# Kernel tuning notes

Measured on AMD Instinct MI355X. Metric: run time of the kernel, lower is better.

Reference implementation:

```python
import jax, jax.numpy as jnp
import numpy as np

EMBED_DIM = 1024
NUM_HEADS = 16
HEAD_DIM = EMBED_DIM // NUM_HEADS
B, T = 4, 2048


def setup_inputs() -> dict:
    key = jax.random.key(0)
    ks = jax.random.split(key, 5)
    s = 0.02
    return {
        "x": jax.random.normal(ks[0], (B, T, EMBED_DIM), dtype=jnp.float32),
        "W_qkv": jax.random.normal(ks[1], (EMBED_DIM, 3 * EMBED_DIM), dtype=jnp.float32) * s,
        "b_qkv": jnp.zeros((3 * EMBED_DIM,), dtype=jnp.float32),
        "W_proj": jax.random.normal(ks[2], (EMBED_DIM, EMBED_DIM), dtype=jnp.float32) * s,
        "b_proj": jnp.zeros((EMBED_DIM,), dtype=jnp.float32),
    }


def reference(x, W_qkv, b_qkv, W_proj, b_proj):
    # Dropout disabled (eval mode) for deterministic reference.
    Bsz, Tlen, C = x.shape
    qkv = x @ W_qkv + b_qkv                          # [B,T,3C]
    q, k, v = jnp.split(qkv, 3, axis=-1)
    def heads(t):  # [B,T,C] -> [B,H,T,Dh]
        return t.reshape(Bsz, Tlen, NUM_HEADS, HEAD_DIM).transpose(0, 2, 1, 3)
    q, k, v = heads(q), heads(k), heads(v)
    scale = HEAD_DIM ** -0.5
    wei = jnp.einsum("bhqd,bhkd->bhqk", q, k) * scale  # [B,H,T,T]
    causal = jnp.tril(jnp.ones((Tlen, Tlen), dtype=bool))
    wei = jnp.where(causal[None, None], wei, -jnp.inf)
    wei = jax.nn.softmax(wei, axis=-1)
    out = jnp.einsum("bhqk,bhkd->bhqd", wei, v)        # [B,H,T,Dh]
    out = out.transpose(0, 2, 1, 3).reshape(Bsz, Tlen, C)
    return out @ W_proj + b_proj
```

## Files before the change

kernel.cpp:

```cpp
#include <hip/hip_runtime.h>

#define DEV __device__ __forceinline__

using u16 = unsigned short;
using u32 = unsigned int;
typedef __attribute__((ext_vector_type(8)))  short  short8;
typedef __attribute__((ext_vector_type(8)))  u16    ushort8;
typedef __attribute__((ext_vector_type(4)))  float  f32x4;
typedef __attribute__((ext_vector_type(16))) float  f32x16;

constexpr int BB = 4;
constexpr int TT = 2048;
constexpr int CC = 1024;
constexpr int HH = 16;
constexpr int DD = 64;
constexpr int MM = BB * TT;
constexpr int N1 = 3 * CC;

DEV u16 f2bf(float f) {
    unsigned u = __float_as_uint(f);
    unsigned r = (u + 0x7FFFu + ((u >> 16) & 1u)) >> 16;
    return (u16)r;
}

DEV u32 cvtpk(float lo, float hi) {
    u32 r;
    asm("v_cvt_pk_bf16_f32 %0, %1, %2" : "=v"(r) : "v"(lo), "v"(hi));
    return r;
}

DEV void gload_lds16(const void* g, void* l) {
    __builtin_amdgcn_global_load_lds((const __attribute__((address_space(1))) void*)g,
                                     (__attribute__((address_space(3))) void*)l,
                                     16, 0, 0);
}

__global__ void k_cvt_x(const float* __restrict__ src, u16* __restrict__ dst) {
    int i = (blockIdx.x * 256 + threadIdx.x) * 8;
    f32x4 a = *(const f32x4*)(src + i);
    f32x4 b = *(const f32x4*)(src + i + 4);
    ushort8 u;
    u[0] = f2bf(a[0]); u[1] = f2bf(a[1]); u[2] = f2bf(a[2]); u[3] = f2bf(a[3]);
    u[4] = f2bf(b[0]); u[5] = f2bf(b[1]); u[6] = f2bf(b[2]); u[7] = f2bf(b[3]);
    *(ushort8*)(dst + i) = u;
}

__global__ void k_transpose_cvt(const float* __restrict__ src, u16* __restrict__ dst,
                                int Kd, int Nd) {
    size_t o = ((size_t)blockIdx.x * 256 + threadIdx.x) * 8;
    int n  = (int)(o / Kd);
    int k0 = (int)(o % Kd);
    ushort8 u;
#pragma unroll
    for (int i = 0; i < 8; ++i)
        u[i] = f2bf(src[(size_t)(k0 + i) * Nd + n]);
    *(ushort8*)(dst + o) = u;
}

DEV void gemm_mainloop(const u16* __restrict__ Ag, const u16* __restrict__ Bg,
                       u16* As, u16* Bs, f32x4 acc[4][4]) {
    const int tid = threadIdx.x, lane = tid & 63, wid = tid >> 6;
    const int wr = wid >> 1, wc = wid & 1;
#pragma unroll 1
    for (int kt = 0; kt < 1024; kt += 32) {
        __syncthreads();
#pragma unroll
        for (int p = 0; p < 2; ++p) {
            int cb = p * 256 + wid * 64;
            int chunk = cb + lane;
            int row = chunk >> 2, kc = chunk & 3;
            gload_lds16(Ag + (size_t)row * 1024 + kt + kc * 8, As + cb * 8);
            gload_lds16(Bg + (size_t)row * 1024 + kt + kc * 8, Bs + cb * 8);
        }
        __syncthreads();
        short8 aF[4], bF[4];
#pragma unroll
        for (int m = 0; m < 4; ++m)
            aF[m] = *(const short8*)&As[(wr * 64 + m * 16 + (lane & 15)) * 32 + (lane >> 4) * 8];
#pragma unroll
        for (int n = 0; n < 4; ++n)
            bF[n] = *(const short8*)&Bs[(wc * 64 + n * 16 + (lane & 15)) * 32 + (lane >> 4) * 8];
#pragma unroll
        for (int m = 0; m < 4; ++m)
#pragma unroll
            for (int n = 0; n < 4; ++n)
                acc[m][n] = __builtin_amdgcn_mfma_f32_16x16x32_bf16(aF[m], bF[n], acc[m][n], 0, 0, 0);
    }
}

__global__ __launch_bounds__(256) void k_gemm_qkv(const u16* __restrict__ xb,
                                                  const u16* __restrict__ wt,
                                                  const float* __restrict__ bqkv,
                                                  u16* __restrict__ qb,
                                                  u16* __restrict__ kb,
                                                  u16* __restrict__ vtb) {
    __shared__ u16 As[4096], Bs[4096];
    f32x4 acc[4][4];
#pragma unroll
    for (int m = 0; m < 4; ++m)
#pragma unroll
        for (int n = 0; n < 4; ++n) acc[m][n] = (f32x4){0.f, 0.f, 0.f, 0.f};
    const int rowBase = blockIdx.x * 128, colBase = blockIdx.y * 128;
    gemm_mainloop(xb + (size_t)rowBase * 1024, wt + (size_t)colBase * 1024, As, Bs, acc);
    const int lane = threadIdx.x & 63, wid = threadIdx.x >> 6;
    const int wr = wid >> 1, wc = wid & 1;
#pragma unroll
    for (int n = 0; n < 4; ++n) {
        int gn = colBase + wc * 64 + n * 16 + (lane & 15);
        float bias = bqkv[gn];
        int which = gn >> 10, cc = gn & 1023, hh = cc >> 6, d = cc & 63;
#pragma unroll
        for (int m = 0; m < 4; ++m) {
#pragma unroll
            for (int r = 0; r < 4; ++r) {
                int gm = rowBase + wr * 64 + m * 16 + (lane >> 4) * 4 + r;
                int b = gm >> 11, t = gm & 2047;
                float val = acc[m][n][r] + bias;
                if (which == 0)
                    qb[(((size_t)b * HH + hh) * TT + t) * DD + d] = f2bf(val * 0.125f);
                else if (which == 1)
                    kb[(((size_t)b * HH + hh) * TT + t) * DD + d] = f2bf(val);
                else
                    vtb[(((size_t)b * HH + hh) * DD + d) * TT + t] = f2bf(val);
            }
        }
    }
}

__global__ __launch_bounds__(256) void k_gemm_proj(const u16* __restrict__ ob,
                                                   const u16* __restrict__ wt,
                                                   const float* __restrict__ bproj,
                                                   float* __restrict__ out) {
    __shared__ u16 As[4096], Bs[4096];
    f32x4 acc[4][4];
#pragma unroll
    for (int m = 0; m < 4; ++m)
#pragma unroll
        for (int n = 0; n < 4; ++n) acc[m][n] = (f32x4){0.f, 0.f, 0.f, 0.f};
    const int rowBase = blockIdx.x * 128, colBase = blockIdx.y * 128;
    gemm_mainloop(ob + (size_t)rowBase * 1024, wt + (size_t)colBase * 1024, As, Bs, acc);
    const int lane = threadIdx.x & 63, wid = threadIdx.x >> 6;
    const int wr = wid >> 1, wc = wid & 1;
#pragma unroll
    for (int n = 0; n < 4; ++n) {
        int gn = colBase + wc * 64 + n * 16 + (lane & 15);
        float bias = bproj[gn];
#pragma unroll
        for (int m = 0; m < 4; ++m) {
#pragma unroll
            for (int r = 0; r < 4; ++r) {
                int gm = rowBase + wr * 64 + m * 16 + (lane >> 4) * 4 + r;
                out[(size_t)gm * 1024 + gn] = acc[m][n][r] + bias;
            }
        }
    }
}

__global__ __launch_bounds__(256) void k_attn2(const u16* __restrict__ qb,
                                               const u16* __restrict__ kb,
                                               const u16* __restrict__ vtb,
                                               u16* __restrict__ ob) {
    __shared__ u16 Kt[2][4096];
    __shared__ u16 Vs[2][4096];

    const int tid = threadIdx.x, lane = tid & 63, w = tid >> 6;
    const int h = lane >> 5, l31 = lane & 31;
    const int bh = blockIdx.x;
    const int qi = 15 - blockIdx.y;
    const size_t hb = (size_t)bh * (TT * DD);
    const int qw = qi * 128 + w * 32;
    const int nt_blk = 2 * qi + 2;
    const int nt_w = (qw >> 6) + 1;
    const int cb = tid & ~63;

    short8 qf[4];
#pragma unroll
    for (int df = 0; df < 4; ++df)
        qf[df] = *(const short8*)(qb + hb + (size_t)(qw + l31) * DD + df * 16 + h * 8);

    f32x16 o0, o1;
#pragma unroll
    for (int r = 0; r < 16; ++r) { o0[r] = 0.f; o1[r] = 0.f; }
    float mrun = -1e30f, lrun = 0.f;

#pragma unroll
    for (int part = 0; part < 2; ++part) {
        int c = part * 256 + tid;
        int row = c >> 3, sw = (c & 7) ^ (row & 7);
        gload_lds16(kb  + hb + (size_t)row * DD + sw * 8,      &Kt[0][(part * 256 + cb) * 8]);
        gload_lds16(vtb + hb + (size_t)row * TT + sw * 8,      &Vs[0][(part * 256 + cb) * 8]);
    }

    int cur = 0;
    for (int j = 0; j < nt_blk; ++j) {
        asm volatile("s_waitcnt vmcnt(0)" ::: "memory");
        __syncthreads();
        if (j + 1 < nt_blk) {
            const int jb = j + 1, nb = cur ^ 1;
#pragma unroll
            for (int part = 0; part < 2; ++part) {
                int c = part * 256 + tid;
                int row = c >> 3, sw = (c & 7) ^ (row & 7);
                gload_lds16(kb  + hb + (size_t)(jb * 64 + row) * DD + sw * 8, &Kt[nb][(part * 256 + cb) * 8]);
                gload_lds16(vtb + hb + (size_t)row * TT + jb * 64 + sw * 8,   &Vs[nb][(part * 256 + cb) * 8]);
            }
        }
        if (j < nt_w) {
            f32x16 s0, s1;
#pragma unroll
            for (int r = 0; r < 16; ++r) { s0[r] = 0.f; s1[r] = 0.f; }
            __builtin_amdgcn_s_setprio(1);
#pragma unroll
            for (int df = 0; df < 4; ++df) {
                int colsw = df * 2 + h;
                int sw = (colsw ^ (l31 & 7)) * 8;
                short8 k0 = *(const short8*)&Kt[cur][l31 * 64 + sw];
                short8 k1 = *(const short8*)&Kt[cur][(l31 + 32) * 64 + sw];
                s0 = __builtin_amdgcn_mfma_f32_32x32x16_bf16(k0, qf[df], s0, 0, 0, 0);
                s1 = __builtin_amdgcn_mfma_f32_32x32x16_bf16(k1, qf[df], s1, 0, 0, 0);
            }
            __builtin_amdgcn_s_setprio(0);

            if (j == nt_w - 1) {
                int qrel = qw + l31 - j * 64;
#pragma unroll
                for (int r = 0; r < 16; ++r) {
                    int kk = (r & 3) + 8 * (r >> 2) + 4 * h;
                    if (kk      > qrel) s0[r] = -1e30f;
                    if (kk + 32 > qrel) s1[r] = -1e30f;
                }
            }

            float pm = -1e30f;
#pragma unroll
            for (int r = 0; r < 16; ++r) pm = fmaxf(pm, fmaxf(s0[r], s1[r]));
            pm = fmaxf(pm, __shfl_xor(pm, 32));
            if (!__all(pm <= mrun + 8.f)) {
                float mnew = fmaxf(mrun, pm);
                float sc = __expf(mrun - mnew);
                mrun = mnew;
                lrun *= sc;
#pragma unroll
                for (int r = 0; r < 16; ++r) {
                    float scr = __shfl(sc, (r & 3) + 8 * (r >> 2) + 4 * h);
                    o0[r] *= scr; o1[r] *= scr;
                }
            }
            float sum = 0.f;
#pragma unroll
            for (int r = 0; r < 16; ++r) {
                float p0 = __expf(s0[r] - mrun); s0[r] = p0; sum += p0;
                float p1 = __expf(s1[r] - mrun); s1[r] = p1; sum += p1;
            }
            sum += __shfl_xor(sum, 32);
            lrun += sum;

            __builtin_amdgcn_s_setprio(1);
#pragma unroll
            for (int f = 0; f < 4; ++f) {
                const f32x16& P = (f >= 2) ? s1 : s0;
                u32 A0, A1, B0, B1;
                if (f & 1) { A0 = cvtpk(P[8],  P[9]);  A1 = cvtpk(P[10], P[11]);
                             B0 = cvtpk(P[12], P[13]); B1 = cvtpk(P[14], P[15]); }
                else       { A0 = cvtpk(P[0],  P[1]);  A1 = cvtpk(P[2],  P[3]);
                             B0 = cvtpk(P[4],  P[5]);  B1 = cvtpk(P[6],  P[7]);  }
                u32 U0 = h ? B0 : A0, U1 = h ? B1 : A1;
                u32 V0 = h ? A0 : B0, V1 = h ? A1 : B1;
                u32 W0 = (u32)__shfl_xor((int)V0, 32);
                u32 W1 = (u32)__shfl_xor((int)V1, 32);
                union { u32 u[4]; short8 s; } pa;
                pa.u[0] = h ? W0 : U0; pa.u[1] = h ? W1 : U1;
                pa.u[2] = h ? U0 : W0; pa.u[3] = h ? U1 : W1;
#pragma unroll
                for (int dt = 0; dt < 2; ++dt) {
                    int row = dt * 32 + l31;
                    short8 vf = *(const short8*)&Vs[cur][row * 64 + (((f * 2 + h) ^ (row & 7)) * 8)];
                    if (dt == 0) o0 = __builtin_amdgcn_mfma_f32_32x32x16_bf16(pa.s, vf, o0, 0, 0, 0);
                    else         o1 = __builtin_amdgcn_mfma_f32_32x32x16_bf16(pa.s, vf, o1, 0, 0, 0);
                }
            }
            __builtin_amdgcn_s_setprio(0);
        }
        cur ^= 1;
    }

    const int b = bh >> 4, head = bh & 15;
    float linv = 1.f / lrun;
#pragma unroll
    for (int r = 0; r < 16; ++r) {
        float li = __shfl(linv, (r & 3) + 8 * (r >> 2) + 4 * h);
        int q = qw + (r & 3) + 8 * (r >> 2) + 4 * h;
        size_t rb = ((size_t)(b * TT + q)) * CC + head * 64;
        ob[rb + l31]      = f2bf(o0[r] * li);
        ob[rb + 32 + l31] = f2bf(o1[r] * li);
    }
}

extern "C" void kernel_launch(void* const* d_in, const int* in_sizes, int n_in,
                              void* d_out, int out_size, void* d_ws, size_t ws_size,
                              hipStream_t stream) {
    const float* x     = (const float*)d_in[0];
    const float* Wqkv  = (const float*)d_in[1];
    const float* bqkv  = (const float*)d_in[2];
    const float* Wproj = (const float*)d_in[3];
    const float* bproj = (const float*)d_in[4];
    float* out = (float*)d_out;

    char* ws = (char*)d_ws;
    u16* xb    = (u16*)(ws + 0);
    u16* wqkvT = (u16*)(ws + 16777216);
    u16* wprojT= (u16*)(ws + 23068672);
    u16* qb    = (u16*)(ws + 25165824);
    u16* kb    = (u16*)(ws + 41943040);
    u16* vtb   = (u16*)(ws + 58720256);
    u16* ob    = xb;

    k_cvt_x<<<dim3(MM * CC / (256 * 8)), 256, 0, stream>>>(x, xb);
    k_transpose_cvt<<<dim3(N1 * CC / (256 * 8)), 256, 0, stream>>>(Wqkv, wqkvT, CC, N1);
    k_transpose_cvt<<<dim3(CC * CC / (256 * 8)), 256, 0, stream>>>(Wproj, wprojT, CC, CC);
    k_gemm_qkv<<<dim3(MM / 128, N1 / 128), 256, 0, stream>>>(xb, wqkvT, bqkv, qb, kb, vtb);
    k_attn2<<<dim3(BB * HH, TT / 128), 256, 0, stream>>>(qb, kb, vtb, ob);
    k_gemm_proj<<<dim3(MM / 128, CC / 128), 256, 0, stream>>>(ob, wprojT, bproj, out);
}
```

Baseline: 309.5 us.

## Double-buffer GEMM LDS staging, swizzle tiles, tile weight transpose, vectorize V store

```diff
diff --git a/kernel.cpp b/kernel.cpp
--- a/kernel.cpp
+++ b/kernel.cpp
@@ -6,6 +6,7 @@
 using u32 = unsigned int;
 typedef __attribute__((ext_vector_type(8)))  short  short8;
 typedef __attribute__((ext_vector_type(8)))  u16    ushort8;
+typedef __attribute__((ext_vector_type(4)))  u16    us4;
 typedef __attribute__((ext_vector_type(4)))  float  f32x4;
 typedef __attribute__((ext_vector_type(16))) float  f32x16;
 
@@ -45,46 +46,67 @@
     *(ushort8*)(dst + i) = u;
 }
 
-__global__ void k_transpose_cvt(const float* __restrict__ src, u16* __restrict__ dst,
-                                int Kd, int Nd) {
-    size_t o = ((size_t)blockIdx.x * 256 + threadIdx.x) * 8;
-    int n  = (int)(o / Kd);
-    int k0 = (int)(o % Kd);
-    ushort8 u;
-#pragma unroll
-    for (int i = 0; i < 8; ++i)
-        u[i] = f2bf(src[(size_t)(k0 + i) * Nd + n]);
-    *(ushort8*)(dst + o) = u;
-}
-
-DEV void gemm_mainloop(const u16* __restrict__ Ag, const u16* __restrict__ Bg,
-                       u16* As, u16* Bs, f32x4 acc[4][4]) {
+__global__ __launch_bounds__(256) void k_transpose_cvt2(const float* __restrict__ src,
+                                                        u16* __restrict__ dst,
+                                                        int Kd, int Nd) {
+    __shared__ u16 tile[64][66];
+    const int t = threadIdx.x;
+    const int k0 = blockIdx.y * 64, n0 = blockIdx.x * 64;
+    const int c = t & 63, r0 = (t >> 6) * 16;
+#pragma unroll
+    for (int i = 0; i < 16; ++i)
+        tile[r0 + i][c] = f2bf(src[(size_t)(k0 + r0 + i) * Nd + n0 + c]);
+    __syncthreads();
+    const int kc = (t & 7) * 8, nn = t >> 3;
+#pragma unroll
+    for (int h = 0; h < 2; ++h) {
+        int n = nn + h * 32;
+        ushort8 v;
+#pragma unroll
+        for (int j = 0; j < 8; ++j) v[j] = tile[kc + j][n];
+        *(ushort8*)(dst + (size_t)(n0 + n) * Kd + k0 + kc) = v;
+    }
+}
+
+DEV void stage_tile(const u16* __restrict__ Ag, const u16* __restrict__ Bg, int kt,
+                    u16* As, u16* Bs, int lane, int wid) {
+#pragma unroll
+    for (int p = 0; p < 2; ++p) {
+        int cb = p * 256 + wid * 64;
+        int chunk = cb + lane;
+        int row = chunk >> 2, kc = chunk & 3;
+        gload_lds16(Ag + (size_t)row * 1024 + kt + kc * 8, As + cb * 8);
+        gload_lds16(Bg + (size_t)row * 1024 + kt + kc * 8, Bs + cb * 8);
+    }
+}
+
+DEV void gemm_mainloop2(const u16* __restrict__ Ag, const u16* __restrict__ Bg,
+                        u16 (*As)[4096], u16 (*Bs)[4096], f32x4 acc[4][4]) {
     const int tid = threadIdx.x, lane = tid & 63, wid = tid >> 6;
     const int wr = wid >> 1, wc = wid & 1;
+    stage_tile(Ag, Bg, 0, As[0], Bs[0], lane, wid);
+    int cur = 0;
 #pragma unroll 1
     for (int kt = 0; kt < 1024; kt += 32) {
+        asm volatile("s_waitcnt vmcnt(0)" ::: "memory");
         __syncthreads();
-#pragma unroll
-        for (int p = 0; p < 2; ++p) {
-            int cb = p * 256 + wid * 64;
-            int chunk = cb + lane;
-            int row = chunk >> 2, kc = chunk & 3;
-            gload_lds16(Ag + (size_t)row * 1024 + kt + kc * 8, As + cb * 8);
-            gload_lds16(Bg + (size_t)row * 1024 + kt + kc * 8, Bs + cb * 8);
-        }
-        __syncthreads();
+        if (kt + 32 < 1024)
+            stage_tile(Ag, Bg, kt + 32, As[cur ^ 1], Bs[cur ^ 1], lane, wid);
         short8 aF[4], bF[4];
 #pragma unroll
         for (int m = 0; m < 4; ++m)
-            aF[m] = *(const short8*)&As[(wr * 64 + m * 16 + (lane & 15)) * 32 + (lane >> 4) * 8];
+            aF[m] = *(const short8*)&As[cur][(wr * 64 + m * 16 + (lane & 15)) * 32 + (lane >> 4) * 8];
 #pragma unroll
         for (int n = 0; n < 4; ++n)
-            bF[n] = *(const short8*)&Bs[(wc * 64 + n * 16 + (lane & 15)) * 32 + (lane >> 4) * 8];
+            bF[n] = *(const short8*)&Bs[cur][(wc * 64 + n * 16 + (lane & 15)) * 32 + (lane >> 4) * 8];
+        __builtin_amdgcn_s_setprio(1);
 #pragma unroll
         for (int m = 0; m < 4; ++m)
 #pragma unroll
             for (int n = 0; n < 4; ++n)
                 acc[m][n] = __builtin_amdgcn_mfma_f32_16x16x32_bf16(aF[m], bF[n], acc[m][n], 0, 0, 0);
+        __builtin_amdgcn_s_setprio(0);
+        cur ^= 1;
     }
 }
 
@@ -94,14 +116,16 @@
                                                   u16* __restrict__ qb,
                                                   u16* __restrict__ kb,
                                                   u16* __restrict__ vtb) {
-    __shared__ u16 As[4096], Bs[4096];
+    __shared__ u16 As[2][4096], Bs[2][4096];
     f32x4 acc[4][4];
 #pragma unroll
     for (int m = 0; m < 4; ++m)
 #pragma unroll
         for (int n = 0; n < 4; ++n) acc[m][n] = (f32x4){0.f, 0.f, 0.f, 0.f};
-    const int rowBase = blockIdx.x * 128, colBase = blockIdx.y * 128;
-    gemm_mainloop(xb + (size_t)rowBase * 1024, wt + (size_t)colBase * 1024, As, Bs, acc);
+    const int orig = blockIdx.y * 64 + blockIdx.x;
+    const int swz = (orig & 7) * 192 + (orig >> 3);
+    const int rowBase = (swz & 63) * 128, colBase = (swz >> 6) * 128;
+    gemm_mainloop2(xb + (size_t)rowBase * 1024, wt + (size_t)colBase * 1024, As, Bs, acc);
     const int lane = threadIdx.x & 63, wid = threadIdx.x >> 6;
     const int wr = wid >> 1, wc = wid & 1;
 #pragma unroll
@@ -109,19 +133,28 @@
         int gn = colBase + wc * 64 + n * 16 + (lane & 15);
         float bias = bqkv[gn];
         int which = gn >> 10, cc = gn & 1023, hh = cc >> 6, d = cc & 63;
-#pragma unroll
-        for (int m = 0; m < 4; ++m) {
-#pragma unroll
-            for (int r = 0; r < 4; ++r) {
-                int gm = rowBase + wr * 64 + m * 16 + (lane >> 4) * 4 + r;
+        if (which == 2) {
+            u16* vdst = vtb + ((size_t)hh * DD + d) * TT;
+#pragma unroll
+            for (int m = 0; m < 4; ++m) {
+                int gm = rowBase + wr * 64 + m * 16 + (lane >> 4) * 4;
                 int b = gm >> 11, t = gm & 2047;
-                float val = acc[m][n][r] + bias;
-                if (which == 0)
-                    qb[(((size_t)b * HH + hh) * TT + t) * DD + d] = f2bf(val * 0.125f);
-                else if (which == 1)
-                    kb[(((size_t)b * HH + hh) * TT + t) * DD + d] = f2bf(val);
-                else
-                    vtb[(((size_t)b * HH + hh) * DD + d) * TT + t] = f2bf(val);
+                us4 pv;
+#pragma unroll
+                for (int r = 0; r < 4; ++r) pv[r] = f2bf(acc[m][n][r] + bias);
+                *(us4*)(vdst + (size_t)b * (HH * DD * TT) + t) = pv;
+            }
+        } else {
+            u16* dst = (which == 0 ? qb : kb);
+            float sc = (which == 0) ? 0.125f : 1.0f;
+#pragma unroll
+            for (int m = 0; m < 4; ++m) {
+#pragma unroll
+                for (int r = 0; r < 4; ++r) {
+                    int gm = rowBase + wr * 64 + m * 16 + (lane >> 4) * 4 + r;
+                    int b = gm >> 11, t = gm & 2047;
+                    dst[(((size_t)b * HH + hh) * TT + t) * DD + d] = f2bf((acc[m][n][r] + bias) * sc);
+                }
             }
         }
     }
@@ -131,14 +164,16 @@
                                                    const u16* __restrict__ wt,
                                                    const float* __restrict__ bproj,
                                                    float* __restrict__ out) {
-    __shared__ u16 As[4096], Bs[4096];
+    __shared__ u16 As[2][4096], Bs[2][4096];
     f32x4 acc[4][4];
 #pragma unroll
     for (int m = 0; m < 4; ++m)
 #pragma unroll
         for (int n = 0; n < 4; ++n) acc[m][n] = (f32x4){0.f, 0.f, 0.f, 0.f};
-    const int rowBase = blockIdx.x * 128, colBase = blockIdx.y * 128;
-    gemm_mainloop(ob + (size_t)rowBase * 1024, wt + (size_t)colBase * 1024, As, Bs, acc);
+    const int orig = blockIdx.y * 64 + blockIdx.x;
+    const int swz = (orig & 7) * 64 + (orig >> 3);
+    const int rowBase = (swz & 63) * 128, colBase = (swz >> 6) * 128;
+    gemm_mainloop2(ob + (size_t)rowBase * 1024, wt + (size_t)colBase * 1024, As, Bs, acc);
     const int lane = threadIdx.x & 63, wid = threadIdx.x >> 6;
     const int wr = wid >> 1, wc = wid & 1;
 #pragma unroll
@@ -316,8 +351,8 @@
     u16* ob    = xb;
 
     k_cvt_x<<<dim3(MM * CC / (256 * 8)), 256, 0, stream>>>(x, xb);
-    k_transpose_cvt<<<dim3(N1 * CC / (256 * 8)), 256, 0, stream>>>(Wqkv, wqkvT, CC, N1);
-    k_transpose_cvt<<<dim3(CC * CC / (256 * 8)), 256, 0, stream>>>(Wproj, wprojT, CC, CC);
+    k_transpose_cvt2<<<dim3(N1 / 64, CC / 64), 256, 0, stream>>>(Wqkv, wqkvT, CC, N1);
+    k_transpose_cvt2<<<dim3(CC / 64, CC / 64), 256, 0, stream>>>(Wproj, wprojT, CC, CC);
     k_gemm_qkv<<<dim3(MM / 128, N1 / 128), 256, 0, stream>>>(xb, wqkvT, bqkv, qb, kb, vtb);
     k_attn2<<<dim3(BB * HH, TT / 128), 256, 0, stream>>>(qb, kb, vtb, ob);
     k_gemm_proj<<<dim3(MM / 128, CC / 128), 256, 0, stream>>>(ob, wprojT, bproj, out);
```

After: 290.4 us. 1.07x faster.
